# Optimization experiments

Measured on AMD Instinct MI355X. Metric: run time of the kernel, lower is better.

The kernel has to match this reference:

```python
import jax, jax.numpy as jnp
import numpy as np

L, H, C, D, B, OUT = 3, 4, 128, 128, 64, 128  # layers, heads, out_ch per head, in_dim, graphs, out_dim
NEG_SLOPE = 0.2
EPS = 1e-5


def _layernorm(x, g, b):
    mu = x.mean(-1, keepdims=True)
    var = ((x - mu) ** 2).mean(-1, keepdims=True)
    return (x - mu) * jax.lax.rsqrt(var + EPS) * g + b


def setup_inputs() -> dict:
    key = jax.random.key(0)
    ks = jax.random.split(key, 20)
    N, E = 50000, 400000
    x = jax.random.normal(ks[0], (N, D), jnp.float32)
    edge_index = jax.random.randint(ks[1], (2, E), 0, N, jnp.int64)
    batch = jnp.sort(jax.random.randint(ks[2], (N,), 0, B, jnp.int64))
    s = 1.0 / np.sqrt(D)
    inp = dict(x=x, edge_index=edge_index, batch=batch)
    inp["Wl"] = jax.random.normal(ks[3], (L, H, C, D), jnp.float32) * s
    inp["bl"] = jnp.zeros((L, H, C), jnp.float32)
    inp["Wr"] = jax.random.normal(ks[4], (L, H, C, D), jnp.float32) * s
    inp["br"] = jnp.zeros((L, H, C), jnp.float32)
    inp["att"] = jax.random.normal(ks[5], (L, H, C), jnp.float32) * (1.0 / np.sqrt(C))
    inp["conv_bias"] = jnp.zeros((L, C), jnp.float32)
    inp["ln_gamma"] = jnp.ones((L, C), jnp.float32)
    inp["ln_beta"] = jnp.zeros((L, C), jnp.float32)
    inp["W1"] = jax.random.normal(ks[6], (2 * C, C), jnp.float32) * (1.0 / np.sqrt(C))
    inp["b1"] = jnp.zeros((2 * C,), jnp.float32)
    inp["W2"] = jax.random.normal(ks[7], (OUT, 2 * C), jnp.float32) * (1.0 / np.sqrt(2 * C))
    inp["b2"] = jnp.zeros((OUT,), jnp.float32)
    inp["og"] = jnp.ones((OUT,), jnp.float32)
    inp["ob"] = jnp.zeros((OUT,), jnp.float32)
    return inp


def reference(x, edge_index, batch, Wl, bl, Wr, br, att, conv_bias, ln_gamma, ln_beta, W1, b1, W2, b2, og, ob):
    N = x.shape[0]
    loops = jnp.arange(N, dtype=edge_index.dtype)
    src = jnp.concatenate([edge_index[0], loops])  # [E+N]
    dst = jnp.concatenate([edge_index[1], loops])
    h = x  # input_proj is Identity (node_feat_dim == hidden_dim)
    for l in range(L):
        xl = jnp.einsum('nd,hcd->nhc', h, Wl[l]) + bl[l]  # [N,H,C]
        xr = jnp.einsum('nd,hcd->nhc', h, Wr[l]) + br[l]
        e = jax.nn.leaky_relu(xl[src] + xr[dst], NEG_SLOPE)  # [E+N,H,C]
        logits = jnp.einsum('ehc,hc->eh', e, att[l])  # [E+N,H]
        m = jax.ops.segment_max(logits, dst, num_segments=N)  # [N,H]
        p = jnp.exp(logits - m[dst])
        denom = jax.ops.segment_sum(p, dst, num_segments=N)
        alpha = p / denom[dst]  # segment softmax (self loops guarantee denom>0)
        out = jax.ops.segment_sum(xl[src] * alpha[:, :, None], dst, num_segments=N)  # [N,H,C]
        out = out.mean(axis=1) + conv_bias[l]  # concat=False -> mean over heads
        out = jax.nn.relu(_layernorm(out, ln_gamma[l], ln_beta[l]))
        h = h + out  # residual
    # global mean pool
    sums = jax.ops.segment_sum(h, batch, num_segments=B)
    cnt = jax.ops.segment_sum(jnp.ones((N,), h.dtype), batch, num_segments=B)
    g = sums / jnp.maximum(cnt, 1.0)[:, None]
    # MLP head + out norm
    g = jax.nn.gelu(g @ W1.T + b1, approximate=False) @ W2.T + b2
    return _layernorm(g, og, ob)
```

## Files before the change

kernel.cpp:

```cpp
#include <hip/hip_runtime.h>
#include <hip/hip_bf16.h>

typedef __bf16 bf16x8 __attribute__((ext_vector_type(8)));
typedef float f32x4 __attribute__((ext_vector_type(4)));
typedef float f32x2 __attribute__((ext_vector_type(2)));
typedef unsigned char u8;

#define EPS 1e-5f

static __device__ __forceinline__ int lower_bound_i(const int* __restrict__ arr, int n, int val) {
  int lo = 0, hi = n;
  while (lo < hi) { int mid = (lo + hi) >> 1; if (arr[mid] < val) lo = mid + 1; else hi = mid; }
  return lo;
}

template <int CTRL>
static __device__ __forceinline__ float dpp_add(float x) {
  int s = __builtin_amdgcn_mov_dpp(__float_as_int(x), CTRL, 0xF, 0xF, true);
  return x + __int_as_float(s);
}
static __device__ __forceinline__ float row16_reduce(float t) {
  t = dpp_add<0xB1>(t);
  t = dpp_add<0x4E>(t);
  t = dpp_add<0x141>(t);
  t = dpp_add<0x140>(t);
  return t;
}

static __device__ __forceinline__ u8 f32_to_fp8(float v) {
  int pk = __builtin_amdgcn_cvt_pk_fp8_f32(v, v, 0, false);
  return (u8)(pk & 0xFF);
}

__global__ void detect_dtypes(const unsigned* __restrict__ xw, const unsigned* __restrict__ eiw,
                              int* __restrict__ flags) {
  __shared__ int s_bf16, s_i64nz;
  int t = threadIdx.x;
  if (t == 0) { s_bf16 = 0; s_i64nz = 0; }
  __syncthreads();
  unsigned w = xw[t * 97];
  unsigned lo = w & 0xFFFFu;
  unsigned e = (lo >> 7) & 0xFF;
  int looks_bf16 = (lo == 0u) || (e >= 0x6A && e <= 0x86);
  atomicAdd(&s_bf16, looks_bf16);
  int k = t * 1031;
  int nz = (eiw[2 * k + 1] != 0u) ? 1 : 0;
  atomicAdd(&s_i64nz, nz);
  __syncthreads();
  if (t == 0) {
    flags[0] = (s_bf16 >= 192) ? 1 : 0;
    flags[1] = (s_i64nz == 0) ? 1 : 0;
  }
}

__global__ void canon_x(const void* __restrict__ src, float* __restrict__ h_f32,
                        __bf16* __restrict__ h_bf, int n, const int* __restrict__ flags) {
  int i = blockIdx.x * blockDim.x + threadIdx.x;
  if (i >= n) return;
  float v;
  if (flags[0]) v = (float)((const __bf16*)src)[i];
  else          v = ((const float*)src)[i];
  h_f32[i] = v;
  h_bf[i] = (__bf16)v;
}

struct ParamDesc { const void* src[12]; int off[13]; };

__global__ void canon_params(ParamDesc pd, float* __restrict__ dst, const int* __restrict__ flags,
                             int total) {
  int i = blockIdx.x * blockDim.x + threadIdx.x;
  if (i >= total) return;
  int s = 0;
#pragma unroll
  for (int k = 1; k < 12; k++) if (i >= pd.off[k]) s = k;
  int j = i - pd.off[s];
  const void* sp = pd.src[s];
  dst[i] = flags[0] ? (float)((const __bf16*)sp)[j] : ((const float*)sp)[j];
}

__global__ void canon_bf16(const void* __restrict__ src, __bf16* __restrict__ dst, int n,
                           const int* __restrict__ flags) {
  int i = blockIdx.x * blockDim.x + threadIdx.x;
  if (i >= n) return;
  if (flags[0]) dst[i] = ((const __bf16*)src)[i];
  else          dst[i] = (__bf16)((const float*)src)[i];
}

__global__ void canon_ints(const void* __restrict__ ei_src, const void* __restrict__ bat_src,
                           int* __restrict__ ei32, int* __restrict__ bat32,
                           int* __restrict__ deg, int E, int N, const int* __restrict__ flags) {
  int i = blockIdx.x * blockDim.x + threadIdx.x;
  int total = 2 * E + N;
  if (i >= total) return;
  int i64 = flags[1];
  if (i < 2 * E) {
    int v = i64 ? (int)((const long long*)ei_src)[i] : ((const int*)ei_src)[i];
    ei32[i] = v;
    if (i >= E) atomicAdd(&deg[v], 1);
  } else {
    int j = i - 2 * E;
    int v = i64 ? (int)((const long long*)bat_src)[j] : ((const int*)bat_src)[j];
    bat32[j] = v;
    atomicAdd(&deg[j], 1);
  }
}

__global__ __launch_bounds__(256) void block_sums(const int* __restrict__ deg,
                                                  int* __restrict__ bsum, int N) {
  __shared__ int sh[256];
  int i = blockIdx.x * 256 + threadIdx.x;
  int t = threadIdx.x;
  sh[t] = (i < N) ? deg[i] : 0;
  __syncthreads();
  for (int off = 128; off > 0; off >>= 1) {
    if (t < off) sh[t] += sh[t + off];
    __syncthreads();
  }
  if (t == 0) bsum[blockIdx.x] = sh[0];
}

__global__ __launch_bounds__(256) void scan_bsums(const int* __restrict__ bsum,
                                                  int* __restrict__ bpref, int nblocks,
                                                  int* __restrict__ offs, int N) {
  __shared__ int sh[256];
  int t = threadIdx.x;
  int carry = 0;
  for (int base = 0; base < nblocks; base += 256) {
    int idx = base + t;
    int v = (idx < nblocks) ? bsum[idx] : 0;
    sh[t] = v;
    __syncthreads();
    for (int off = 1; off < 256; off <<= 1) {
      int u = (t >= off) ? sh[t - off] : 0;
      __syncthreads();
      sh[t] += u;
      __syncthreads();
    }
    if (idx < nblocks) bpref[idx] = carry + sh[t] - v;
    carry += sh[255];
    __syncthreads();
  }
  if (t == 0) offs[N] = carry;
}

__global__ __launch_bounds__(256) void write_offs(const int* __restrict__ deg,
                                                  const int* __restrict__ bpref,
                                                  int* __restrict__ offs,
                                                  int* __restrict__ cursor, int N) {
  __shared__ int sh[256];
  int i = blockIdx.x * 256 + threadIdx.x;
  int t = threadIdx.x;
  int v = (i < N) ? deg[i] : 0;
  sh[t] = v;
  __syncthreads();
  for (int off = 1; off < 256; off <<= 1) {
    int u = (t >= off) ? sh[t - off] : 0;
    __syncthreads();
    sh[t] += u;
    __syncthreads();
  }
  if (i < N) {
    int ex = bpref[blockIdx.x] + sh[t] - v;
    offs[i] = ex;
    cursor[i] = ex;
  }
}

__global__ void fill_csr(const int* __restrict__ ei, int E, int N,
                         int* __restrict__ cursor, int* __restrict__ csr_src) {
  int e = blockIdx.x * blockDim.x + threadIdx.x;
  if (e >= E + N) return;
  int s, d;
  if (e < E) { s = ei[e]; d = ei[E + e]; } else { s = e - E; d = e - E; }
  int pos = atomicAdd(&cursor[d], 1);
  csr_src[pos] = s;
}

__global__ __launch_bounds__(256) void gemm_xlr(
    const __bf16* __restrict__ A, const __bf16* __restrict__ Wl,
    const __bf16* __restrict__ Wr, const float* __restrict__ bl,
    const float* __restrict__ br, u8* __restrict__ out8, int Nrows) {
  __shared__ __bf16 As[128][72];
  __shared__ __bf16 Bs[128][72];
  const int jb = blockIdx.y;
  const __bf16* Wbase = (jb < 4) ? (Wl + (size_t)jb * 128 * 128) : (Wr + (size_t)(jb - 4) * 128 * 128);
  const float* biasbase = (jb < 4) ? (bl + jb * 128) : (br + (jb - 4) * 128);
  const int row0 = blockIdx.x * 128;
  const int tid = threadIdx.x;
  const int lane = tid & 63, wave = tid >> 6;
  const int wm = wave >> 1, wn = wave & 1;

  f32x4 zero4 = {0.f, 0.f, 0.f, 0.f};
  f32x4 acc[4][4];
#pragma unroll
  for (int mi = 0; mi < 4; mi++)
#pragma unroll
    for (int ni = 0; ni < 4; ni++) acc[mi][ni] = zero4;

  for (int kc = 0; kc < 2; kc++) {
    __syncthreads();
#pragma unroll
    for (int p = 0; p < 4; p++) {
      int r = (tid >> 3) + p * 32;
      int cg = (tid & 7) * 8;
      int gr = row0 + r;
      bf16x8 av;
      if (gr < Nrows) av = *(const bf16x8*)(A + (size_t)gr * 128 + kc * 64 + cg);
      else {
#pragma unroll
        for (int j = 0; j < 8; j++) av[j] = (__bf16)0.0f;
      }
      *(bf16x8*)(&As[r][cg]) = av;
      bf16x8 bv = *(const bf16x8*)(Wbase + (size_t)r * 128 + kc * 64 + cg);
      *(bf16x8*)(&Bs[r][cg]) = bv;
    }
    __syncthreads();
#pragma unroll
    for (int s = 0; s < 2; s++) {
      bf16x8 af[4], bfr[4];
      int kofs = s * 32 + ((lane >> 4) * 8);
#pragma unroll
      for (int i = 0; i < 4; i++) {
        af[i]  = *(const bf16x8*)(&As[wm * 64 + i * 16 + (lane & 15)][kofs]);
        bfr[i] = *(const bf16x8*)(&Bs[wn * 64 + i * 16 + (lane & 15)][kofs]);
      }
#pragma unroll
      for (int mi = 0; mi < 4; mi++)
#pragma unroll
        for (int ni = 0; ni < 4; ni++)
          acc[mi][ni] = __builtin_amdgcn_mfma_f32_16x16x32_bf16(af[mi], bfr[ni], acc[mi][ni], 0, 0, 0);
    }
  }
#pragma unroll
  for (int mi = 0; mi < 4; mi++) {
#pragma unroll
    for (int ni = 0; ni < 4; ni++) {
      int col_l = wn * 64 + ni * 16 + (lane & 15);
      int gj = jb * 128 + col_l;
      float bias = biasbase[col_l];
#pragma unroll
      for (int r = 0; r < 4; r++) {
        int row_l = wm * 64 + mi * 16 + (lane >> 4) * 4 + r;
        int gr = row0 + row_l;
        if (gr < Nrows) out8[(size_t)gr * 1024 + gj] = f32_to_fp8(acc[mi][ni][r] + bias);
      }
    }
  }
}

__global__ __launch_bounds__(256) void gat_fused(
    const u8* __restrict__ comb8, const float* __restrict__ att,
    const int* __restrict__ offs, const int* __restrict__ csr_src,
    const float* __restrict__ conv_bias, const float* __restrict__ gamma,
    const float* __restrict__ beta, float* __restrict__ h_f32,
    __bf16* __restrict__ h_bf, int N) {
  int wid = blockIdx.x * 4 + (threadIdx.x >> 6);
  int lane = threadIdx.x & 63;
  if (wid >= N) return;
  int n = wid;
  f32x2 xr2[4], at2[4];
  uint2 wr = *(const uint2*)(comb8 + (size_t)n * 1024 + 512 + lane * 8);
  xr2[0] = __builtin_amdgcn_cvt_pk_f32_fp8(wr.x, false);
  xr2[1] = __builtin_amdgcn_cvt_pk_f32_fp8(wr.x, true);
  xr2[2] = __builtin_amdgcn_cvt_pk_f32_fp8(wr.y, false);
  xr2[3] = __builtin_amdgcn_cvt_pk_f32_fp8(wr.y, true);
  float4 a0 = *(const float4*)(att + lane * 8);
  float4 a1 = *(const float4*)(att + lane * 8 + 4);
  at2[0] = f32x2{a0.x, a0.y}; at2[1] = f32x2{a0.z, a0.w};
  at2[2] = f32x2{a1.x, a1.y}; at2[3] = f32x2{a1.z, a1.w};

  int off0 = offs[n], off1 = offs[n + 1];
  float l = 0.f;
  f32x2 acc2[4];
#pragma unroll
  for (int j = 0; j < 4; j++) acc2[j] = f32x2{0.f, 0.f};

  const u8* lane_base = comb8 + lane * 8;

  auto process = [&](uint2 w) {
    f32x2 x2[4];
    x2[0] = __builtin_amdgcn_cvt_pk_f32_fp8(w.x, false);
    x2[1] = __builtin_amdgcn_cvt_pk_f32_fp8(w.x, true);
    x2[2] = __builtin_amdgcn_cvt_pk_f32_fp8(w.y, false);
    x2[3] = __builtin_amdgcn_cvt_pk_f32_fp8(w.y, true);
    f32x2 t2 = f32x2{0.f, 0.f};
#pragma unroll
    for (int j = 0; j < 4; j++) {
      f32x2 z = x2[j] + xr2[j];
      f32x2 lz = __builtin_elementwise_max(z, 0.2f * z);
      t2 = t2 + lz * at2[j];
    }
    float t = t2[0] + t2[1];
    t = row16_reduce(t);
    t = fminf(fmaxf(t, -60.f), 60.f);
    float p = __expf(t);
    l += p;
    f32x2 p2 = f32x2{p, p};
#pragma unroll
    for (int j = 0; j < 4; j++) acc2[j] = acc2[j] + p2 * x2[j];
  };

  int pos = off0;
  for (; pos + 2 <= off1; pos += 2) {
    int s0 = csr_src[pos], s1 = csr_src[pos + 1];
    uint2 wa = *(const uint2*)(lane_base + (size_t)s0 * 1024);
    uint2 wb = *(const uint2*)(lane_base + (size_t)s1 * 1024);
    process(wa);
    process(wb);
  }
  if (pos < off1) {
    int s0 = csr_src[pos];
    uint2 wa = *(const uint2*)(lane_base + (size_t)s0 * 1024);
    process(wa);
  }

  float invl = 1.0f / fmaxf(l, 1e-30f);
  float acc[8];
#pragma unroll
  for (int j = 0; j < 4; j++) {
    acc[2 * j]     = acc2[j][0] * invl;
    acc[2 * j + 1] = acc2[j][1] * invl;
  }
#pragma unroll
  for (int j = 0; j < 8; j++) {
    acc[j] += __shfl_xor(acc[j], 16);
    acc[j] += __shfl_xor(acc[j], 32);
  }
  int c0 = (lane & 15) * 8;
  float v[8];
  float s = 0.f, s2 = 0.f;
#pragma unroll
  for (int j = 0; j < 8; j++) {
    v[j] = acc[j] * 0.25f + conv_bias[c0 + j];
    s += v[j]; s2 += v[j] * v[j];
  }
  s = row16_reduce(s);
  s2 = row16_reduce(s2);
  float mu = s * (1.f / 128.f);
  float var = fmaxf(s2 * (1.f / 128.f) - mu * mu, 0.f);
  float rs = rsqrtf(var + EPS);
  if (lane < 16) {
    float4 o0, o1;
    bf16x8 hb;
    float hn[8];
#pragma unroll
    for (int j = 0; j < 8; j++) {
      float o = (v[j] - mu) * rs * gamma[c0 + j] + beta[c0 + j];
      o = o > 0.f ? o : 0.f;
      hn[j] = h_f32[(size_t)n * 128 + c0 + j] + o;
      hb[j] = (__bf16)hn[j];
    }
    o0.x = hn[0]; o0.y = hn[1]; o0.z = hn[2]; o0.w = hn[3];
    o1.x = hn[4]; o1.y = hn[5]; o1.z = hn[6]; o1.w = hn[7];
    *(float4*)(h_f32 + (size_t)n * 128 + c0) = o0;
    *(float4*)(h_f32 + (size_t)n * 128 + c0 + 4) = o1;
    *(bf16x8*)(h_bf + (size_t)n * 128 + c0) = hb;
  }
}

__global__ __launch_bounds__(128) void pool(const float* __restrict__ h_f32,
                                            const int* __restrict__ batch, int N,
                                            float* __restrict__ g_sum) {
  int g = blockIdx.x >> 3, slice = blockIdx.x & 7;
  int c = threadIdx.x;
  int r0 = lower_bound_i(batch, N, g);
  int r1 = lower_bound_i(batch, N, g + 1);
  int len = r1 - r0;
  if (len <= 0) return;
  int per = (len + 7) / 8;
  int s0 = r0 + slice * per;
  int s1 = min(s0 + per, r1);
  if (s0 >= s1) return;
  float acc = 0.f;
  for (int r = s0; r < s1; r++) acc += h_f32[(size_t)r * 128 + c];
  atomicAdd(&g_sum[g * 128 + c], acc);
}

__global__ __launch_bounds__(256) void mlp_head(
    const float* __restrict__ g_sum, const int* __restrict__ batch, int N,
    const float* __restrict__ W1, const float* __restrict__ b1,
    const float* __restrict__ W2, const float* __restrict__ b2,
    const float* __restrict__ og, const float* __restrict__ ob,
    void* __restrict__ outv, const int* __restrict__ flags) {
  __shared__ float gld[128];
  __shared__ float hid[256];
  __shared__ float olds[128];
  __shared__ float red[2];
  int b = blockIdx.x, t = threadIdx.x;
  int r0 = lower_bound_i(batch, N, b);
  int r1 = lower_bound_i(batch, N, b + 1);
  int len = r1 - r0;
  float cntf = (float)(len < 1 ? 1 : len);
  if (t < 128) gld[t] = g_sum[b * 128 + t] / cntf;
  __syncthreads();
  float sacc = b1[t];
  for (int d = 0; d < 128; d++) sacc = fmaf(gld[d], W1[(size_t)t * 128 + d], sacc);
  hid[t] = 0.5f * sacc * (1.f + erff(sacc * 0.70710678118654752f));
  __syncthreads();
  if (t < 128) {
    float o = b2[t];
    for (int k = 0; k < 256; k++) o = fmaf(hid[k], W2[(size_t)t * 256 + k], o);
    olds[t] = o;
  }
  __syncthreads();
  if (t < 64) {
    float a = olds[t], bb = olds[t + 64];
    float s = a + bb, s2 = a * a + bb * bb;
    for (int off = 32; off; off >>= 1) { s += __shfl_down(s, off); s2 += __shfl_down(s2, off); }
    if (t == 0) { red[0] = s * (1.f / 128.f); red[1] = s2 * (1.f / 128.f); }
  }
  __syncthreads();
  if (t < 128) {
    float mu = red[0];
    float var = fmaxf(red[1] - mu * mu, 0.f);
    float rs = rsqrtf(var + EPS);
    float o = (olds[t] - mu) * rs * og[t] + ob[t];
    if (flags[0]) ((__bf16*)outv)[b * 128 + t] = (__bf16)o;
    else          ((float*)outv)[b * 128 + t] = o;
  }
}

extern "C" void kernel_launch(void* const* d_in, const int* in_sizes, int n_in,
                              void* d_out, int out_size, void* d_ws, size_t ws_size,
                              hipStream_t stream) {
  const int D = 128, B = 64;
  const int N = in_sizes[0] / D;
  const int E = in_sizes[1] / 2;
  const int EN = E + N;
  const int nsb = (N + 255) / 256;

  char* p = (char*)d_ws;
  auto alloc = [&](size_t bytes) {
    char* r = p; p += (bytes + 255) & ~(size_t)255; return (void*)r;
  };
  int* flags     = (int*)alloc(256);
  float* h_f32   = (float*)alloc((size_t)N * 128 * 4);
  __bf16* h_bf   = (__bf16*)alloc((size_t)N * 128 * 2);
  u8* comb8      = (u8*)alloc((size_t)N * 1024);
  int* deg       = (int*)alloc((size_t)N * 4);
  int* offs      = (int*)alloc((size_t)(N + 1) * 4);
  int* cursor    = (int*)alloc((size_t)N * 4);
  int* csr_src   = (int*)alloc((size_t)EN * 4);
  float* g_sum   = (float*)alloc((size_t)B * 128 * 4);
  int* ei32      = (int*)alloc((size_t)2 * E * 4);
  int* bat32     = (int*)alloc((size_t)N * 4);
  int* bsum      = (int*)alloc((size_t)nsb * 4);
  int* bpref     = (int*)alloc((size_t)nsb * 4);
  __bf16* w_bf   = (__bf16*)alloc((size_t)2 * 196608 * 2);
  float* params  = (float*)alloc((size_t)71936 * 4);

  float* bl_c  = params + 0;
  float* br_c  = params + 1536;
  float* att_c = params + 3072;
  float* cb_c  = params + 4608;
  float* g_c   = params + 4992;
  float* b_c   = params + 5376;
  float* W1_c  = params + 5760;
  float* b1_c  = params + 38528;
  float* W2_c  = params + 38784;
  float* b2_c  = params + 71552;
  float* og_c  = params + 71680;
  float* ob_c  = params + 71808;

  detect_dtypes<<<1, 256, 0, stream>>>((const unsigned*)d_in[0], (const unsigned*)d_in[1], flags);

  canon_x<<<(N * 128 + 255) / 256, 256, 0, stream>>>(d_in[0], h_f32, h_bf, N * 128, flags);

  ParamDesc pd;
  const int srcidx[12] = {4, 6, 7, 8, 9, 10, 11, 12, 13, 14, 15, 16};
  const int sizes12[12] = {1536, 1536, 1536, 384, 384, 384, 32768, 256, 32768, 128, 128, 128};
  int cum = 0;
  for (int k = 0; k < 12; k++) { pd.src[k] = d_in[srcidx[k]]; pd.off[k] = cum; cum += sizes12[k]; }
  pd.off[12] = cum;
  canon_params<<<(cum + 255) / 256, 256, 0, stream>>>(pd, params, flags, cum);

  canon_bf16<<<(196608 + 255) / 256, 256, 0, stream>>>(d_in[3], w_bf, 196608, flags);
  canon_bf16<<<(196608 + 255) / 256, 256, 0, stream>>>(d_in[5], w_bf + 196608, 196608, flags);

  hipMemsetAsync(deg, 0, (size_t)N * 4, stream);
  hipMemsetAsync(g_sum, 0, (size_t)B * 128 * 4, stream);

  canon_ints<<<(2 * E + N + 255) / 256, 256, 0, stream>>>(d_in[1], d_in[2], ei32, bat32, deg, E, N, flags);
  block_sums<<<nsb, 256, 0, stream>>>(deg, bsum, N);
  scan_bsums<<<1, 256, 0, stream>>>(bsum, bpref, nsb, offs, N);
  write_offs<<<nsb, 256, 0, stream>>>(deg, bpref, offs, cursor, N);
  fill_csr<<<(EN + 255) / 256, 256, 0, stream>>>(ei32, E, N, cursor, csr_src);

  for (int l = 0; l < 3; l++) {
    gemm_xlr<<<dim3((N + 127) / 128, 8), 256, 0, stream>>>(
        h_bf, w_bf + (size_t)l * 65536, w_bf + 196608 + (size_t)l * 65536,
        bl_c + l * 512, br_c + l * 512, comb8, N);
    gat_fused<<<(N + 3) / 4, 256, 0, stream>>>(comb8, att_c + l * 512, offs, csr_src,
        cb_c + l * 128, g_c + l * 128, b_c + l * 128, h_f32, h_bf, N);
  }
  pool<<<B * 8, 128, 0, stream>>>(h_f32, bat32, N, g_sum);
  mlp_head<<<B, 256, 0, stream>>>(g_sum, bat32, N, W1_c, b1_c, W2_c, b2_c, og_c, ob_c, d_out, flags);
}
```

Measured before the change: 572.3 us.

## Restructure XLR GEMM to keep A tile in registers across head blocks

Measured after the change: 632.3 us. 1.1x slower.

```diff
diff --git a/kernel.cpp b/kernel.cpp
--- a/kernel.cpp
+++ b/kernel.cpp
@@ -173,76 +173,94 @@
   int s, d;
   if (e < E) { s = ei[e]; d = ei[E + e]; } else { s = e - E; d = e - E; }
   int pos = atomicAdd(&cursor[d], 1);
-  csr_src[pos] = s;
+  csr_src[pos] = s * 1024;
 }
 
 __global__ __launch_bounds__(256) void gemm_xlr(
     const __bf16* __restrict__ A, const __bf16* __restrict__ Wl,
     const __bf16* __restrict__ Wr, const float* __restrict__ bl,
     const float* __restrict__ br, u8* __restrict__ out8, int Nrows) {
-  __shared__ __bf16 As[128][72];
-  __shared__ __bf16 Bs[128][72];
-  const int jb = blockIdx.y;
-  const __bf16* Wbase = (jb < 4) ? (Wl + (size_t)jb * 128 * 128) : (Wr + (size_t)(jb - 4) * 128 * 128);
-  const float* biasbase = (jb < 4) ? (bl + jb * 128) : (br + (jb - 4) * 128);
-  const int row0 = blockIdx.x * 128;
+  __shared__ __bf16 As[64][136];
+  __shared__ __bf16 Ws[128][136];
+  const int y = blockIdx.y;
+  const __bf16* Wsel = y ? Wr : Wl;
+  const float* bsel = y ? br : bl;
+  const int row0 = blockIdx.x * 64;
   const int tid = threadIdx.x;
   const int lane = tid & 63, wave = tid >> 6;
-  const int wm = wave >> 1, wn = wave & 1;
-
-  f32x4 zero4 = {0.f, 0.f, 0.f, 0.f};
-  f32x4 acc[4][4];
-#pragma unroll
-  for (int mi = 0; mi < 4; mi++)
-#pragma unroll
-    for (int ni = 0; ni < 4; ni++) acc[mi][ni] = zero4;
-
-  for (int kc = 0; kc < 2; kc++) {
-    __syncthreads();
-#pragma unroll
-    for (int p = 0; p < 4; p++) {
-      int r = (tid >> 3) + p * 32;
-      int cg = (tid & 7) * 8;
-      int gr = row0 + r;
-      bf16x8 av;
-      if (gr < Nrows) av = *(const bf16x8*)(A + (size_t)gr * 128 + kc * 64 + cg);
-      else {
-#pragma unroll
-        for (int j = 0; j < 8; j++) av[j] = (__bf16)0.0f;
+
+#pragma unroll
+  for (int p = 0; p < 4; p++) {
+    int oct = tid + p * 256;
+    int r = oct >> 4, c = (oct & 15) * 8;
+    int gr = row0 + r;
+    bf16x8 av;
+    if (gr < Nrows) av = *(const bf16x8*)(A + (size_t)gr * 128 + c);
+    else {
+#pragma unroll
+      for (int j = 0; j < 8; j++) av[j] = (__bf16)0.0f;
+    }
+    *(bf16x8*)(&As[r][c]) = av;
+  }
+  __syncthreads();
+  bf16x8 af[2][2][4];
+#pragma unroll
+  for (int kc = 0; kc < 2; kc++)
+#pragma unroll
+    for (int s = 0; s < 2; s++) {
+      int kofs = kc * 64 + s * 32 + (lane >> 4) * 8;
+#pragma unroll
+      for (int mi = 0; mi < 4; mi++)
+        af[kc][s][mi] = *(const bf16x8*)(&As[mi * 16 + (lane & 15)][kofs]);
+    }
+
+  for (int j4 = 0; j4 < 4; j4++) {
+    __syncthreads();
+    const __bf16* Wbase = Wsel + (size_t)j4 * 16384;
+#pragma unroll
+    for (int p = 0; p < 8; p++) {
+      int oct = tid + p * 256;
+      int r = oct >> 4, c = (oct & 15) * 8;
+      *(bf16x8*)(&Ws[r][c]) = *(const bf16x8*)(Wbase + (size_t)r * 128 + c);
+    }
+    __syncthreads();
+
+    f32x4 acc[4][2];
+#pragma unroll
+    for (int mi = 0; mi < 4; mi++)
+#pragma unroll
+      for (int ni = 0; ni < 2; ni++) acc[mi][ni] = f32x4{0.f, 0.f, 0.f, 0.f};
+
+#pragma unroll
+    for (int kc = 0; kc < 2; kc++)
+#pragma unroll
+      for (int s = 0; s < 2; s++) {
+        int kofs = kc * 64 + s * 32 + (lane >> 4) * 8;
+        bf16x8 bfr[2];
+#pragma unroll
+        for (int ni = 0; ni < 2; ni++)
+          bfr[ni] = *(const bf16x8*)(&Ws[wave * 32 + ni * 16 + (lane & 15)][kofs]);
+#pragma unroll
+        for (int mi = 0; mi < 4; mi++)
+#pragma unroll
+          for (int ni = 0; ni < 2; ni++)
+            acc[mi][ni] = __builtin_amdgcn_mfma_f32_16x16x32_bf16(af[kc][s][mi], bfr[ni], acc[mi][ni], 0, 0, 0);
       }
-      *(bf16x8*)(&As[r][cg]) = av;
-      bf16x8 bv = *(const bf16x8*)(Wbase + (size_t)r * 128 + kc * 64 + cg);
-      *(bf16x8*)(&Bs[r][cg]) = bv;
-    }
-    __syncthreads();
-#pragma unroll
-    for (int s = 0; s < 2; s++) {
-      bf16x8 af[4], bfr[4];
-      int kofs = s * 32 + ((lane >> 4) * 8);
-#pragma unroll
-      for (int i = 0; i < 4; i++) {
-        af[i]  = *(const bf16x8*)(&As[wm * 64 + i * 16 + (lane & 15)][kofs]);
-        bfr[i] = *(const bf16x8*)(&Bs[wn * 64 + i * 16 + (lane & 15)][kofs]);
-      }
-#pragma unroll
-      for (int mi = 0; mi < 4; mi++)
-#pragma unroll
-        for (int ni = 0; ni < 4; ni++)
-          acc[mi][ni] = __builtin_amdgcn_mfma_f32_16x16x32_bf16(af[mi], bfr[ni], acc[mi][ni], 0, 0, 0);
-    }
-  }
-#pragma unroll
-  for (int mi = 0; mi < 4; mi++) {
-#pragma unroll
-    for (int ni = 0; ni < 4; ni++) {
-      int col_l = wn * 64 + ni * 16 + (lane & 15);
-      int gj = jb * 128 + col_l;
-      float bias = biasbase[col_l];
-#pragma unroll
-      for (int r = 0; r < 4; r++) {
-        int row_l = wm * 64 + mi * 16 + (lane >> 4) * 4 + r;
-        int gr = row0 + row_l;
-        if (gr < Nrows) out8[(size_t)gr * 1024 + gj] = f32_to_fp8(acc[mi][ni][r] + bias);
+
+    int jb = y * 4 + j4;
+#pragma unroll
+    for (int mi = 0; mi < 4; mi++) {
+#pragma unroll
+      for (int ni = 0; ni < 2; ni++) {
+        int col_l = wave * 32 + ni * 16 + (lane & 15);
+        int gj = jb * 128 + col_l;
+        float bias = bsel[j4 * 128 + col_l];
+#pragma unroll
+        for (int r = 0; r < 4; r++) {
+          int row_l = mi * 16 + (lane >> 4) * 4 + r;
+          int gr = row0 + row_l;
+          if (gr < Nrows) out8[(size_t)gr * 1024 + gj] = f32_to_fp8(acc[mi][ni][r] + bias);
+        }
       }
     }
   }
@@ -253,7 +271,7 @@
     const int* __restrict__ offs, const int* __restrict__ csr_src,
     const float* __restrict__ conv_bias, const float* __restrict__ gamma,
     const float* __restrict__ beta, float* __restrict__ h_f32,
-    __bf16* __restrict__ h_bf, int N) {
+    __bf16* __restrict__ h_bf, int N, int store_bf) {
   int wid = blockIdx.x * 4 + (threadIdx.x >> 6);
   int lane = threadIdx.x & 63;
   if (wid >= N) return;
@@ -302,15 +320,15 @@
 
   int pos = off0;
   for (; pos + 2 <= off1; pos += 2) {
-    int s0 = csr_src[pos], s1 = csr_src[pos + 1];
-    uint2 wa = *(const uint2*)(lane_base + (size_t)s0 * 1024);
-    uint2 wb = *(const uint2*)(lane_base + (size_t)s1 * 1024);
+    int b0 = csr_src[pos], b1 = csr_src[pos + 1];
+    uint2 wa = *(const uint2*)(lane_base + (size_t)(unsigned)b0);
+    uint2 wb = *(const uint2*)(lane_base + (size_t)(unsigned)b1);
     process(wa);
     process(wb);
   }
   if (pos < off1) {
-    int s0 = csr_src[pos];
-    uint2 wa = *(const uint2*)(lane_base + (size_t)s0 * 1024);
+    int b0 = csr_src[pos];
+    uint2 wa = *(const uint2*)(lane_base + (size_t)(unsigned)b0);
     process(wa);
   }
 
@@ -354,7 +372,7 @@
     o1.x = hn[4]; o1.y = hn[5]; o1.z = hn[6]; o1.w = hn[7];
     *(float4*)(h_f32 + (size_t)n * 128 + c0) = o0;
     *(float4*)(h_f32 + (size_t)n * 128 + c0 + 4) = o1;
-    *(bf16x8*)(h_bf + (size_t)n * 128 + c0) = hb;
+    if (store_bf) *(bf16x8*)(h_bf + (size_t)n * 128 + c0) = hb;
   }
 }
 
@@ -487,11 +505,11 @@
   fill_csr<<<(EN + 255) / 256, 256, 0, stream>>>(ei32, E, N, cursor, csr_src);
 
   for (int l = 0; l < 3; l++) {
-    gemm_xlr<<<dim3((N + 127) / 128, 8), 256, 0, stream>>>(
+    gemm_xlr<<<dim3((N + 63) / 64, 2), 256, 0, stream>>>(
         h_bf, w_bf + (size_t)l * 65536, w_bf + 196608 + (size_t)l * 65536,
         bl_c + l * 512, br_c + l * 512, comb8, N);
     gat_fused<<<(N + 3) / 4, 256, 0, stream>>>(comb8, att_c + l * 512, offs, csr_src,
-        cb_c + l * 128, g_c + l * 128, b_c + l * 128, h_f32, h_bf, N);
+        cb_c + l * 128, g_c + l * 128, b_c + l * 128, h_f32, h_bf, N, (l < 2) ? 1 : 0);
   }
   pool<<<B * 8, 128, 0, stream>>>(h_f32, bat32, N, g_sum);
   mlp_head<<<B, 256, 0, stream>>>(g_sum, bat32, N, W1_c, b1_c, W2_c, b2_c, og_c, ob_c, d_out, flags);
```

## Switch node projection GEMM to FP8 MFMA with FP8 activations and weights

Applied to the files above, without the earlier changes.

New measurement: 545.6 us. 1.05x faster.

```diff
diff --git a/kernel.cpp b/kernel.cpp
--- a/kernel.cpp
+++ b/kernel.cpp
@@ -1,10 +1,12 @@
 #include <hip/hip_runtime.h>
 #include <hip/hip_bf16.h>
 
+typedef __bf16 bf16x4 __attribute__((ext_vector_type(4)));
 typedef __bf16 bf16x8 __attribute__((ext_vector_type(8)));
 typedef float f32x4 __attribute__((ext_vector_type(4)));
 typedef float f32x2 __attribute__((ext_vector_type(2)));
 typedef unsigned char u8;
+typedef unsigned long long u64;
 
 #define EPS 1e-5f
 
@@ -30,6 +32,11 @@
 static __device__ __forceinline__ u8 f32_to_fp8(float v) {
   int pk = __builtin_amdgcn_cvt_pk_fp8_f32(v, v, 0, false);
   return (u8)(pk & 0xFF);
+}
+static __device__ __forceinline__ unsigned pack4_fp8(float a, float b, float c, float d) {
+  int w = __builtin_amdgcn_cvt_pk_fp8_f32(a, b, 0, false);
+  w = __builtin_amdgcn_cvt_pk_fp8_f32(c, d, w, true);
+  return (unsigned)w;
 }
 
 __global__ void detect_dtypes(const unsigned* __restrict__ xw, const unsigned* __restrict__ eiw,
@@ -54,14 +61,19 @@
 }
 
 __global__ void canon_x(const void* __restrict__ src, float* __restrict__ h_f32,
-                        __bf16* __restrict__ h_bf, int n, const int* __restrict__ flags) {
+                        u8* __restrict__ h8, int n4, const int* __restrict__ flags) {
   int i = blockIdx.x * blockDim.x + threadIdx.x;
-  if (i >= n) return;
-  float v;
-  if (flags[0]) v = (float)((const __bf16*)src)[i];
-  else          v = ((const float*)src)[i];
-  h_f32[i] = v;
-  h_bf[i] = (__bf16)v;
+  if (i >= n4) return;
+  float v0, v1, v2, v3;
+  if (flags[0]) {
+    bf16x4 u = ((const bf16x4*)src)[i];
+    v0 = (float)u[0]; v1 = (float)u[1]; v2 = (float)u[2]; v3 = (float)u[3];
+  } else {
+    float4 u = ((const float4*)src)[i];
+    v0 = u.x; v1 = u.y; v2 = u.z; v3 = u.w;
+  }
+  ((float4*)h_f32)[i] = make_float4(v0, v1, v2, v3);
+  ((unsigned*)h8)[i] = pack4_fp8(v0, v1, v2, v3);
 }
 
 struct ParamDesc { const void* src[12]; int off[13]; };
@@ -78,12 +90,12 @@
   dst[i] = flags[0] ? (float)((const __bf16*)sp)[j] : ((const float*)sp)[j];
 }
 
-__global__ void canon_bf16(const void* __restrict__ src, __bf16* __restrict__ dst, int n,
-                           const int* __restrict__ flags) {
+__global__ void canon_w8(const void* __restrict__ src, u8* __restrict__ dst, int n,
+                         const int* __restrict__ flags) {
   int i = blockIdx.x * blockDim.x + threadIdx.x;
   if (i >= n) return;
-  if (flags[0]) dst[i] = ((const __bf16*)src)[i];
-  else          dst[i] = (__bf16)((const float*)src)[i];
+  float v = flags[0] ? (float)((const __bf16*)src)[i] : ((const float*)src)[i];
+  dst[i] = f32_to_fp8(v);
 }
 
 __global__ void canon_ints(const void* __restrict__ ei_src, const void* __restrict__ bat_src,
@@ -173,64 +185,60 @@
   int s, d;
   if (e < E) { s = ei[e]; d = ei[E + e]; } else { s = e - E; d = e - E; }
   int pos = atomicAdd(&cursor[d], 1);
-  csr_src[pos] = s;
+  csr_src[pos] = s * 1024;
 }
 
 __global__ __launch_bounds__(256) void gemm_xlr(
-    const __bf16* __restrict__ A, const __bf16* __restrict__ Wl,
-    const __bf16* __restrict__ Wr, const float* __restrict__ bl,
+    const u8* __restrict__ A8, const u8* __restrict__ Wl8,
+    const u8* __restrict__ Wr8, const float* __restrict__ bl,
     const float* __restrict__ br, u8* __restrict__ out8, int Nrows) {
-  __shared__ __bf16 As[128][72];
-  __shared__ __bf16 Bs[128][72];
+  __shared__ u64 As[128][19];
+  __shared__ u64 Ws[128][19];
   const int jb = blockIdx.y;
-  const __bf16* Wbase = (jb < 4) ? (Wl + (size_t)jb * 128 * 128) : (Wr + (size_t)(jb - 4) * 128 * 128);
+  const u8* Wbase = (jb < 4) ? (Wl8 + (size_t)jb * 16384) : (Wr8 + (size_t)(jb - 4) * 16384);
   const float* biasbase = (jb < 4) ? (bl + jb * 128) : (br + (jb - 4) * 128);
   const int row0 = blockIdx.x * 128;
   const int tid = threadIdx.x;
   const int lane = tid & 63, wave = tid >> 6;
   const int wm = wave >> 1, wn = wave & 1;
 
-  f32x4 zero4 = {0.f, 0.f, 0.f, 0.f};
+#pragma unroll
+  for (int p = 0; p < 4; p++) {
+    int r = (tid >> 3) + p * 32;
+    int qc = (tid & 7) * 2;
+    int gr = row0 + r;
+    uint4 av = make_uint4(0, 0, 0, 0);
+    if (gr < Nrows) av = *(const uint4*)(A8 + (size_t)gr * 128 + qc * 8);
+    As[r][qc]     = ((u64)av.y << 32) | av.x;
+    As[r][qc + 1] = ((u64)av.w << 32) | av.z;
+    uint4 wv = *(const uint4*)(Wbase + (size_t)r * 128 + qc * 8);
+    Ws[r][qc]     = ((u64)wv.y << 32) | wv.x;
+    Ws[r][qc + 1] = ((u64)wv.w << 32) | wv.z;
+  }
+  __syncthreads();
+
   f32x4 acc[4][4];
 #pragma unroll
   for (int mi = 0; mi < 4; mi++)
 #pragma unroll
-    for (int ni = 0; ni < 4; ni++) acc[mi][ni] = zero4;
-
-  for (int kc = 0; kc < 2; kc++) {
-    __syncthreads();
-#pragma unroll
-    for (int p = 0; p < 4; p++) {
-      int r = (tid >> 3) + p * 32;
-      int cg = (tid & 7) * 8;
-      int gr = row0 + r;
-      bf16x8 av;
-      if (gr < Nrows) av = *(const bf16x8*)(A + (size_t)gr * 128 + kc * 64 + cg);
-      else {
-#pragma unroll
-        for (int j = 0; j < 8; j++) av[j] = (__bf16)0.0f;
-      }
-      *(bf16x8*)(&As[r][cg]) = av;
-      bf16x8 bv = *(const bf16x8*)(Wbase + (size_t)r * 128 + kc * 64 + cg);
-      *(bf16x8*)(&Bs[r][cg]) = bv;
+    for (int ni = 0; ni < 4; ni++) acc[mi][ni] = f32x4{0.f, 0.f, 0.f, 0.f};
+
+#pragma unroll
+  for (int ks = 0; ks < 4; ks++) {
+    int qk = ks * 4 + (lane >> 4);
+    long af[4], bf[4];
+#pragma unroll
+    for (int i = 0; i < 4; i++) {
+      af[i] = (long)As[wm * 64 + i * 16 + (lane & 15)][qk];
+      bf[i] = (long)Ws[wn * 64 + i * 16 + (lane & 15)][qk];
     }
-    __syncthreads();
-#pragma unroll
-    for (int s = 0; s < 2; s++) {
-      bf16x8 af[4], bfr[4];
-      int kofs = s * 32 + ((lane >> 4) * 8);
-#pragma unroll
-      for (int i = 0; i < 4; i++) {
-        af[i]  = *(const bf16x8*)(&As[wm * 64 + i * 16 + (lane & 15)][kofs]);
-        bfr[i] = *(const bf16x8*)(&Bs[wn * 64 + i * 16 + (lane & 15)][kofs]);
-      }
-#pragma unroll
-      for (int mi = 0; mi < 4; mi++)
-#pragma unroll
-        for (int ni = 0; ni < 4; ni++)
-          acc[mi][ni] = __builtin_amdgcn_mfma_f32_16x16x32_bf16(af[mi], bfr[ni], acc[mi][ni], 0, 0, 0);
-    }
-  }
+#pragma unroll
+    for (int mi = 0; mi < 4; mi++)
+#pragma unroll
+      for (int ni = 0; ni < 4; ni++)
+        acc[mi][ni] = __builtin_amdgcn_mfma_f32_16x16x32_fp8_fp8(af[mi], bf[ni], acc[mi][ni], 0, 0, 0);
+  }
+
 #pragma unroll
   for (int mi = 0; mi < 4; mi++) {
 #pragma unroll
@@ -253,7 +261,7 @@
     const int* __restrict__ offs, const int* __restrict__ csr_src,
     const float* __restrict__ conv_bias, const float* __restrict__ gamma,
     const float* __restrict__ beta, float* __restrict__ h_f32,
-    __bf16* __restrict__ h_bf, int N) {
+    u8* __restrict__ h8, int N, int store_fp8) {
   int wid = blockIdx.x * 4 + (threadIdx.x >> 6);
   int lane = threadIdx.x & 63;
   if (wid >= N) return;
@@ -302,15 +310,15 @@
 
   int pos = off0;
   for (; pos + 2 <= off1; pos += 2) {
-    int s0 = csr_src[pos], s1 = csr_src[pos + 1];
-    uint2 wa = *(const uint2*)(lane_base + (size_t)s0 * 1024);
-    uint2 wb = *(const uint2*)(lane_base + (size_t)s1 * 1024);
+    int b0 = csr_src[pos], b1 = csr_src[pos + 1];
+    uint2 wa = *(const uint2*)(lane_base + (size_t)(unsigned)b0);
+    uint2 wb = *(const uint2*)(lane_base + (size_t)(unsigned)b1);
     process(wa);
     process(wb);
   }
   if (pos < off1) {
-    int s0 = csr_src[pos];
-    uint2 wa = *(const uint2*)(lane_base + (size_t)s0 * 1024);
+    int b0 = csr_src[pos];
+    uint2 wa = *(const uint2*)(lane_base + (size_t)(unsigned)b0);
     process(wa);
   }
 
@@ -341,20 +349,23 @@
   float rs = rsqrtf(var + EPS);
   if (lane < 16) {
     float4 o0, o1;
-    bf16x8 hb;
     float hn[8];
 #pragma unroll
     for (int j = 0; j < 8; j++) {
       float o = (v[j] - mu) * rs * gamma[c0 + j] + beta[c0 + j];
       o = o > 0.f ? o : 0.f;
       hn[j] = h_f32[(size_t)n * 128 + c0 + j] + o;
-      hb[j] = (__bf16)hn[j];
     }
     o0.x = hn[0]; o0.y = hn[1]; o0.z = hn[2]; o0.w = hn[3];
     o1.x = hn[4]; o1.y = hn[5]; o1.z = hn[6]; o1.w = hn[7];
     *(float4*)(h_f32 + (size_t)n * 128 + c0) = o0;
     *(float4*)(h_f32 + (size_t)n * 128 + c0 + 4) = o1;
-    *(bf16x8*)(h_bf + (size_t)n * 128 + c0) = hb;
+    if (store_fp8) {
+      uint2 pk;
+      pk.x = pack4_fp8(hn[0], hn[1], hn[2], hn[3]);
+      pk.y = pack4_fp8(hn[4], hn[5], hn[6], hn[7]);
+      *(uint2*)(h8 + (size_t)n * 128 + c0) = pk;
+    }
   }
 }
 
@@ -435,7 +446,7 @@
   };
   int* flags     = (int*)alloc(256);
   float* h_f32   = (float*)alloc((size_t)N * 128 * 4);
-  __bf16* h_bf   = (__bf16*)alloc((size_t)N * 128 * 2);
+  u8* h8         = (u8*)alloc((size_t)N * 128);
   u8* comb8      = (u8*)alloc((size_t)N * 1024);
   int* deg       = (int*)alloc((size_t)N * 4);
   int* offs      = (int*)alloc((size_t)(N + 1) * 4);
@@ -446,7 +457,7 @@
   int* bat32     = (int*)alloc((size_t)N * 4);
   int* bsum      = (int*)alloc((size_t)nsb * 4);
   int* bpref     = (int*)alloc((size_t)nsb * 4);
-  __bf16* w_bf   = (__bf16*)alloc((size_t)2 * 196608 * 2);
+  u8* w8         = (u8*)alloc((size_t)2 * 196608);
   float* params  = (float*)alloc((size_t)71936 * 4);
 
   float* bl_c  = params + 0;
@@ -464,7 +475,7 @@
 
   detect_dtypes<<<1, 256, 0, stream>>>((const unsigned*)d_in[0], (const unsigned*)d_in[1], flags);
 
-  canon_x<<<(N * 128 + 255) / 256, 256, 0, stream>>>(d_in[0], h_f32, h_bf, N * 128, flags);
+  canon_x<<<(N * 32 + 255) / 256, 256, 0, stream>>>(d_in[0], h_f32, h8, N * 32, flags);
 
   ParamDesc pd;
   const int srcidx[12] = {4, 6, 7, 8, 9, 10, 11, 12, 13, 14, 15, 16};
@@ -474,8 +485,8 @@
   pd.off[12] = cum;
   canon_params<<<(cum + 255) / 256, 256, 0, stream>>>(pd, params, flags, cum);
 
-  canon_bf16<<<(196608 + 255) / 256, 256, 0, stream>>>(d_in[3], w_bf, 196608, flags);
-  canon_bf16<<<(196608 + 255) / 256, 256, 0, stream>>>(d_in[5], w_bf + 196608, 196608, flags);
+  canon_w8<<<(196608 + 255) / 256, 256, 0, stream>>>(d_in[3], w8, 196608, flags);
+  canon_w8<<<(196608 + 255) / 256, 256, 0, stream>>>(d_in[5], w8 + 196608, 196608, flags);
 
   hipMemsetAsync(deg, 0, (size_t)N * 4, stream);
   hipMemsetAsync(g_sum, 0, (size_t)B * 128 * 4, stream);
@@ -488,10 +499,10 @@
 
   for (int l = 0; l < 3; l++) {
     gemm_xlr<<<dim3((N + 127) / 128, 8), 256, 0, stream>>>(
-        h_bf, w_bf + (size_t)l * 65536, w_bf + 196608 + (size_t)l * 65536,
+        h8, w8 + (size_t)l * 65536, w8 + 196608 + (size_t)l * 65536,
         bl_c + l * 512, br_c + l * 512, comb8, N);
     gat_fused<<<(N + 3) / 4, 256, 0, stream>>>(comb8, att_c + l * 512, offs, csr_src,
-        cb_c + l * 128, g_c + l * 128, b_c + l * 128, h_f32, h_bf, N);
+        cb_c + l * 128, g_c + l * 128, b_c + l * 128, h_f32, h8, N, (l < 2) ? 1 : 0);
   }
   pool<<<B * 8, 128, 0, stream>>>(h_f32, bat32, N, g_sum);
   mlp_head<<<B, 256, 0, stream>>>(g_sum, bat32, N, W1_c, b1_c, W2_c, b2_c, og_c, ob_c, d_out, flags);
```
